# Optimization experiments

Measured on AMD Instinct MI355X. Metric: run time of the kernel, lower is better.

The kernel has to match this reference:

```python
import jax
import jax.numpy as jnp
import numpy as np


def setup_inputs() -> dict:
    key = jax.random.key(0)
    k1, k2 = jax.random.split(key)
    C, H, W = 21, 1024, 1024
    prediction = jax.random.normal(k1, (C, H, W), dtype=jnp.float32)
    label = jax.random.randint(k2, (C, H, W), 0, 100, dtype=jnp.int32)
    return {"prediction": prediction, "label": label}


def reference(prediction, label):
    C, H, W = prediction.shape
    # label.max(dim=0) -> per-pixel argmax class id, flattened to (N,)
    lbl = jnp.argmax(label, axis=0).reshape(-1)
    # permute(1,2,0).view(-1, C) -> (N, C)
    pred = jnp.transpose(prediction, (1, 2, 0)).reshape(-1, C)

    def per_class(c):
        fg = (lbl == c).astype(pred.dtype)          # (N,) foreground mask
        errors = jnp.abs(fg - pred[:, c])            # (N,)
        order = jnp.argsort(-errors)                 # descending sort perm
        errors_sorted = errors[order]
        fg_sorted = fg[order]
        gts = fg_sorted.sum()
        intersection = gts - jnp.cumsum(fg_sorted)
        union = gts + jnp.cumsum(1.0 - fg_sorted)
        jaccard = 1.0 - intersection / union
        # gradient of Lovasz extension: first-difference of jaccard
        jaccard = jnp.concatenate([jaccard[:1], jaccard[1:] - jaccard[:-1]])
        return jnp.dot(errors_sorted, jaccard)

    losses = jax.vmap(per_class)(jnp.arange(C))
    return losses.mean()
```

## Files before the change

kernel.cpp:

```cpp
#include <hip/hip_runtime.h>

constexpr int NPIX  = 1 << 20;
constexpr int NCLS  = 21;
constexpr int NBINS = 960;
constexpr float RANGE = 8.0f;
constexpr float BIN_SCALE = NBINS / RANGE;
constexpr int NCHUNK = 256;
constexpr int CHUNK_PIX = NPIX / NCHUNK;
constexpr int NGRP = 8;
constexpr int CPG  = NCHUNK / NGRP;

typedef int   iv4 __attribute__((ext_vector_type(4)));
typedef float fv4 __attribute__((ext_vector_type(4)));

__global__ void __launch_bounds__(1024, 4)
k_fused(const iv4* __restrict__ label4, const fv4* __restrict__ pred4,
        unsigned int* __restrict__ part) {
    __shared__ unsigned int sh[NCLS * NBINS];
    const int chunk = blockIdx.x;
    const int t     = threadIdx.x;

    {
        uint4* s4 = (uint4*)sh;
        for (int b = t; b < NCLS * NBINS / 4; b += 1024)
            s4[b] = make_uint4(0u, 0u, 0u, 0u);
    }
    __syncthreads();

    const int q = chunk * (CHUNK_PIX / 4) + t;

    iv4 lv[NCLS];
    #pragma unroll
    for (int c = 0; c < NCLS; ++c)
        lv[c] = label4[(size_t)c * (NPIX / 4) + q];

    int bx = 0, by = 0, bz = 0, bw = 0;
    iv4 best = lv[0];
    #pragma unroll
    for (int c = 1; c < NCLS; ++c) {
        if (lv[c].x > best.x) { best.x = lv[c].x; bx = c; }
        if (lv[c].y > best.y) { best.y = lv[c].y; by = c; }
        if (lv[c].z > best.z) { best.z = lv[c].z; bz = c; }
        if (lv[c].w > best.w) { best.w = lv[c].w; bw = c; }
    }

    fv4 pv[NCLS];
    #pragma unroll
    for (int c = 0; c < NCLS; ++c)
        pv[c] = pred4[(size_t)c * (NPIX / 4) + q];

    #pragma unroll
    for (int c = 0; c < NCLS; ++c) {
        unsigned int* shc = sh + c * NBINS;
        {
            unsigned int fg = (bx == c) ? 1u : 0u;
            float e = fabsf((float)fg - pv[c].x);
            int bin = (int)(e * BIN_SCALE); bin = bin < NBINS - 1 ? bin : NBINS - 1;
            atomicAdd(&shc[bin], 1u | (fg << 16));
        }
        {
            unsigned int fg = (by == c) ? 1u : 0u;
            float e = fabsf((float)fg - pv[c].y);
            int bin = (int)(e * BIN_SCALE); bin = bin < NBINS - 1 ? bin : NBINS - 1;
            atomicAdd(&shc[bin], 1u | (fg << 16));
        }
        {
            unsigned int fg = (bz == c) ? 1u : 0u;
            float e = fabsf((float)fg - pv[c].z);
            int bin = (int)(e * BIN_SCALE); bin = bin < NBINS - 1 ? bin : NBINS - 1;
            atomicAdd(&shc[bin], 1u | (fg << 16));
        }
        {
            unsigned int fg = (bw == c) ? 1u : 0u;
            float e = fabsf((float)fg - pv[c].w);
            int bin = (int)(e * BIN_SCALE); bin = bin < NBINS - 1 ? bin : NBINS - 1;
            atomicAdd(&shc[bin], 1u | (fg << 16));
        }
    }
    __syncthreads();

    uint4* dst = (uint4*)(part + (size_t)chunk * NCLS * NBINS);
    const uint4* src = (const uint4*)sh;
    for (int b = t; b < NCLS * NBINS / 4; b += 1024) dst[b] = src[b];
}

__global__ void k_merge(const unsigned int* __restrict__ part,
                        unsigned long long* __restrict__ part2) {
    int b = blockIdx.x * blockDim.x + threadIdx.x;
    if (b >= NCLS * NBINS) return;
    int g = blockIdx.y;
    unsigned int n = 0, f = 0;
    for (int k = 0; k < CPG; ++k) {
        unsigned int v = part[(size_t)(g * CPG + k) * (NCLS * NBINS) + b];
        n += v & 0xFFFFu;
        f += v >> 16;
    }
    part2[(size_t)g * (NCLS * NBINS) + b] =
        (unsigned long long)n | ((unsigned long long)f << 32);
}

__global__ void __launch_bounds__(1024)
k_scan(const unsigned long long* __restrict__ part2, double* __restrict__ losses) {
    const int c    = blockIdx.x;
    const int t    = threadIdx.x;
    const int lane = t & 63;
    const int wv   = t >> 6;

    const int bin = NBINS - 1 - t;
    unsigned int tn = 0, tf = 0;
    if (t < NBINS) {
        #pragma unroll
        for (int g = 0; g < NGRP; ++g) {
            unsigned long long v =
                part2[(size_t)g * (NCLS * NBINS) + (size_t)c * NBINS + bin];
            tn += (unsigned int)v;
            tf += (unsigned int)(v >> 32);
        }
    }

    unsigned int in_ = tn, if_ = tf;
    #pragma unroll
    for (int off = 1; off < 64; off <<= 1) {
        unsigned int an = __shfl_up(in_, off, 64);
        unsigned int af = __shfl_up(if_, off, 64);
        if (lane >= off) { in_ += an; if_ += af; }
    }

    __shared__ unsigned int swn[16], swf[16];
    if (lane == 63) { swn[wv] = in_; swf[wv] = if_; }
    __syncthreads();

    if (wv == 0 && lane < 16) {
        unsigned int a = swn[lane], b = swf[lane];
        #pragma unroll
        for (int off = 1; off < 16; off <<= 1) {
            unsigned int an = __shfl_up(a, off, 64);
            unsigned int af = __shfl_up(b, off, 64);
            if (lane >= off) { a += an; b += af; }
        }
        swn[lane] = a; swf[lane] = b;
    }
    __syncthreads();

    const unsigned int G = swf[15];
    unsigned int i = in_ - tn + (wv ? swn[wv - 1] : 0u);
    unsigned int F = if_ - tf + (wv ? swf[wv - 1] : 0u);

    double acc = 0.0;
    if (tn) {
        double jprev = (i > 0) ? (double)i / (double)(G + i - F) : 0.0;
        unsigned int i2 = i + tn, F2 = F + tf;
        double jhi = (double)i2 / (double)(G + i2 - F2);
        acc = ((bin + 0.5) * (double)(RANGE / NBINS)) * (jhi - jprev);
    }

    #pragma unroll
    for (int off = 32; off > 0; off >>= 1) acc += __shfl_down(acc, off, 64);
    __shared__ double sd[16];
    if (lane == 0) sd[wv] = acc;
    __syncthreads();
    if (t == 0) {
        double s = 0.0;
        #pragma unroll
        for (int k = 0; k < 16; ++k) s += sd[k];
        losses[c] = s;
    }
}

__global__ void k_final(const double* __restrict__ losses, float* __restrict__ out) {
    if (threadIdx.x == 0 && blockIdx.x == 0) {
        double s = 0.0;
        for (int c = 0; c < NCLS; ++c) s += losses[c];
        out[0] = (float)(s / NCLS);
    }
}

extern "C" void kernel_launch(void* const* d_in, const int* in_sizes, int n_in,
                              void* d_out, int out_size, void* d_ws, size_t ws_size,
                              hipStream_t stream) {
    const float* pred  = (const float*)d_in[0];
    const int*   label = (const int*)d_in[1];
    float* out = (float*)d_out;

    char* ws = (char*)d_ws;
    unsigned int* part = (unsigned int*)ws;
    size_t off = (size_t)NCHUNK * NCLS * NBINS * 4;
    unsigned long long* part2 = (unsigned long long*)(ws + off);
    off += (size_t)NGRP * NCLS * NBINS * 8;
    double* losses = (double*)(ws + off);

    k_fused<<<NCHUNK, 1024, 0, stream>>>((const iv4*)label, (const fv4*)pred, part);
    dim3 mgrid((NCLS * NBINS + 255) / 256, NGRP);
    k_merge<<<mgrid, 256, 0, stream>>>(part, part2);
    k_scan<<<NCLS, 1024, 0, stream>>>(part2, losses);
    k_final<<<1, 64, 0, stream>>>(losses, out);
}
```

Baseline: 45.25 us.

## Halve histogram bins, use 512-thread chunks, fuse merge into scan kernel

Cuts the histogram resolution from 960 to 480 bins and doubles the chunk count so each 512-thread block handles the same pixels per thread. The separate merge kernel is removed: the scan kernel now reads all 512 per-chunk partial histograms directly and sums them, which drops one launch and the intermediate buffer. The price is coarser bins, which loosens the loss approximation, and 21 scan blocks that each walk 512 strided loads serially, which may be slow.

```diff
diff --git a/kernel.cpp b/kernel.cpp
--- a/kernel.cpp
+++ b/kernel.cpp
@@ -2,18 +2,17 @@
 
 constexpr int NPIX  = 1 << 20;
 constexpr int NCLS  = 21;
-constexpr int NBINS = 960;
+constexpr int NBINS = 480;
 constexpr float RANGE = 8.0f;
 constexpr float BIN_SCALE = NBINS / RANGE;
-constexpr int NCHUNK = 256;
+constexpr int NCHUNK = 512;
 constexpr int CHUNK_PIX = NPIX / NCHUNK;
-constexpr int NGRP = 8;
-constexpr int CPG  = NCHUNK / NGRP;
+constexpr int BLK = 512;
 
 typedef int   iv4 __attribute__((ext_vector_type(4)));
 typedef float fv4 __attribute__((ext_vector_type(4)));
 
-__global__ void __launch_bounds__(1024, 4)
+__global__ void __launch_bounds__(BLK, 8)
 k_fused(const iv4* __restrict__ label4, const fv4* __restrict__ pred4,
         unsigned int* __restrict__ part) {
     __shared__ unsigned int sh[NCLS * NBINS];
@@ -22,7 +21,7 @@
 
     {
         uint4* s4 = (uint4*)sh;
-        for (int b = t; b < NCLS * NBINS / 4; b += 1024)
+        for (int b = t; b < NCLS * NBINS / 4; b += BLK)
             s4[b] = make_uint4(0u, 0u, 0u, 0u);
     }
     __syncthreads();
@@ -81,26 +80,11 @@
 
     uint4* dst = (uint4*)(part + (size_t)chunk * NCLS * NBINS);
     const uint4* src = (const uint4*)sh;
-    for (int b = t; b < NCLS * NBINS / 4; b += 1024) dst[b] = src[b];
+    for (int b = t; b < NCLS * NBINS / 4; b += BLK) dst[b] = src[b];
 }
 
-__global__ void k_merge(const unsigned int* __restrict__ part,
-                        unsigned long long* __restrict__ part2) {
-    int b = blockIdx.x * blockDim.x + threadIdx.x;
-    if (b >= NCLS * NBINS) return;
-    int g = blockIdx.y;
-    unsigned int n = 0, f = 0;
-    for (int k = 0; k < CPG; ++k) {
-        unsigned int v = part[(size_t)(g * CPG + k) * (NCLS * NBINS) + b];
-        n += v & 0xFFFFu;
-        f += v >> 16;
-    }
-    part2[(size_t)g * (NCLS * NBINS) + b] =
-        (unsigned long long)n | ((unsigned long long)f << 32);
-}
-
-__global__ void __launch_bounds__(1024)
-k_scan(const unsigned long long* __restrict__ part2, double* __restrict__ losses) {
+__global__ void __launch_bounds__(512)
+k_mergescan(const unsigned int* __restrict__ part, double* __restrict__ losses) {
     const int c    = blockIdx.x;
     const int t    = threadIdx.x;
     const int lane = t & 63;
@@ -109,12 +93,12 @@
     const int bin = NBINS - 1 - t;
     unsigned int tn = 0, tf = 0;
     if (t < NBINS) {
-        #pragma unroll
-        for (int g = 0; g < NGRP; ++g) {
-            unsigned long long v =
-                part2[(size_t)g * (NCLS * NBINS) + (size_t)c * NBINS + bin];
-            tn += (unsigned int)v;
-            tf += (unsigned int)(v >> 32);
+        const unsigned int* p = part + (size_t)c * NBINS + bin;
+        #pragma unroll 8
+        for (int k = 0; k < NCHUNK; ++k) {
+            unsigned int v = p[(size_t)k * (NCLS * NBINS)];
+            tn += v & 0xFFFFu;
+            tf += v >> 16;
         }
     }
 
@@ -126,14 +110,14 @@
         if (lane >= off) { in_ += an; if_ += af; }
     }
 
-    __shared__ unsigned int swn[16], swf[16];
+    __shared__ unsigned int swn[8], swf[8];
     if (lane == 63) { swn[wv] = in_; swf[wv] = if_; }
     __syncthreads();
 
-    if (wv == 0 && lane < 16) {
+    if (wv == 0 && lane < 8) {
         unsigned int a = swn[lane], b = swf[lane];
         #pragma unroll
-        for (int off = 1; off < 16; off <<= 1) {
+        for (int off = 1; off < 8; off <<= 1) {
             unsigned int an = __shfl_up(a, off, 64);
             unsigned int af = __shfl_up(b, off, 64);
             if (lane >= off) { a += an; b += af; }
@@ -142,7 +126,7 @@
     }
     __syncthreads();
 
-    const unsigned int G = swf[15];
+    const unsigned int G = swf[7];
     unsigned int i = in_ - tn + (wv ? swn[wv - 1] : 0u);
     unsigned int F = if_ - tf + (wv ? swf[wv - 1] : 0u);
 
@@ -156,13 +140,13 @@
 
     #pragma unroll
     for (int off = 32; off > 0; off >>= 1) acc += __shfl_down(acc, off, 64);
-    __shared__ double sd[16];
+    __shared__ double sd[8];
     if (lane == 0) sd[wv] = acc;
     __syncthreads();
     if (t == 0) {
         double s = 0.0;
         #pragma unroll
-        for (int k = 0; k < 16; ++k) s += sd[k];
+        for (int k = 0; k < 8; ++k) s += sd[k];
         losses[c] = s;
     }
 }
@@ -185,13 +169,9 @@
     char* ws = (char*)d_ws;
     unsigned int* part = (unsigned int*)ws;
     size_t off = (size_t)NCHUNK * NCLS * NBINS * 4;
-    unsigned long long* part2 = (unsigned long long*)(ws + off);
-    off += (size_t)NGRP * NCLS * NBINS * 8;
     double* losses = (double*)(ws + off);
 
-    k_fused<<<NCHUNK, 1024, 0, stream>>>((const iv4*)label, (const fv4*)pred, part);
-    dim3 mgrid((NCLS * NBINS + 255) / 256, NGRP);
-    k_merge<<<mgrid, 256, 0, stream>>>(part, part2);
-    k_scan<<<NCLS, 1024, 0, stream>>>(part2, losses);
+    k_fused<<<NCHUNK, BLK, 0, stream>>>((const iv4*)label, (const fv4*)pred, part);
+    k_mergescan<<<NCLS, 512, 0, stream>>>(part, losses);
     k_final<<<1, 64, 0, stream>>>(losses, out);
 }
```

Result: slower. 73.87 us (+63.3%).
